# Kernel tuning notes

Hardware: AMD Instinct MI355X
Metric: run time of the kernel (lower is better)

## Reference

```python
import jax, jax.numpy as jnp
import numpy as np

K = 128          # scratch_keys_dim
A = 200          # actions_dim == scratch_values_dim
NP1 = 4          # n_pointers + 1
MAXLEN = 50      # PositionalEncoding max_len
H = K * NP1      # GRU hidden = 512


def make_pe(max_len, d):
    # Standard transformer sinusoidal positional encoding (used as scratch keys).
    pos = jnp.arange(max_len, dtype=jnp.float32)[:, None]
    div = jnp.exp(jnp.arange(0, d, 2, dtype=jnp.float32) * (-np.log(10000.0) / d))
    pe = jnp.zeros((max_len, d), jnp.float32)
    pe = pe.at[:, 0::2].set(jnp.sin(pos * div))
    pe = pe.at[:, 1::2].set(jnp.cos(pos * div))
    return pe


def setup_inputs() -> dict:
    key = jax.random.key(0)
    ks = jax.random.split(key, 12)
    B, INS, ACT = 256, 8, 33
    IN_V, OUT_V = 16, 8
    return {
        "instructions": jax.random.randint(ks[0], (INS, B), 0, IN_V, dtype=jnp.int32),
        "true_actions": jax.random.randint(ks[1], (ACT, B), 0, OUT_V, dtype=jnp.int32),
        "initial_scratch_value": jax.random.normal(ks[2], (A,), jnp.float32),
        "program_emb": jax.random.normal(ks[3], (IN_V, 200), jnp.float32) * 0.05,
        "primitive_emb": jax.random.normal(ks[4], (IN_V, A), jnp.float32) * 0.05,
        "gate_w": jax.random.normal(ks[5], (1, K), jnp.float32) * 0.05,
        "gate_b": jnp.zeros((1,), jnp.float32),
        "w_ih": jax.random.normal(ks[6], (3 * H, 1), jnp.float32) * 0.05,
        "w_hh": jax.random.normal(ks[7], (3 * H, H), jnp.float32) * 0.05,
        "b_ih": jnp.zeros((3 * H,), jnp.float32),
        "b_hh": jnp.zeros((3 * H,), jnp.float32),
        "out_w": jax.random.normal(ks[8], (OUT_V, A), jnp.float32) * 0.05,
        "out_b": jnp.zeros((OUT_V,), jnp.float32),
    }


def reference(instructions, true_actions, initial_scratch_value, program_emb,
              primitive_emb, gate_w, gate_b, w_ih, w_hh, b_ih, b_hh, out_w, out_b):
    B = instructions.shape[1]
    padded_true = true_actions[1:]              # drop BOS row, [L, B]
    L = padded_true.shape[0]                    # max_len == max_program_steps
    pe = make_pe(MAXLEN, K)
    SK = pe[:L]                                 # scratch keys [L, K] (same for all batch)
    h0 = jnp.broadcast_to(jnp.tile(pe[0], (NP1,)), (B, H))
    sv0 = jnp.broadcast_to(initial_scratch_value, (B, L, A))

    # GRU input is always zeros(B,1); compute input-side gates once.
    gi = jnp.zeros((B, 1), jnp.float32) @ w_ih.T + b_ih   # [B, 3H]

    def gru(h):
        gh = h @ w_hh.T + b_hh
        r = jax.nn.sigmoid(gi[:, :H] + gh[:, :H])
        z = jax.nn.sigmoid(gi[:, H:2 * H] + gh[:, H:2 * H])
        n = jnp.tanh(gi[:, 2 * H:] + r * gh[:, 2 * H:])
        return (1.0 - z) * n + z * h

    def word_step(carry, word):
        h, sv = carry
        prim = primitive_emb[word]              # [B, A]
        _prog = program_emb[word]               # computed but unused in original forward

        def step(c, _):
            h, sv = c
            read_p = h[:, K:2 * K]              # [B, K]
            write_p = h[:, 2 * K:3 * K]
            gate = jax.nn.sigmoid(h[:, 3 * K:4 * K] @ gate_w.T + gate_b)   # [B, 1]
            # soft read: dot-product attention over scratch keys
            read_attn = jax.nn.softmax(read_p @ SK.T, axis=-1)             # [B, L]
            read_val = jnp.einsum('bl,bla->ba', read_attn, sv)             # [B, A]
            new_val = gate * prim + (1.0 - gate) * read_val                # [B, A]
            # soft write: convex blend of new value into every slot
            wm = jax.nn.softmax(write_p @ SK.T, axis=-1)[:, :, None]       # [B, L, 1]
            sv = wm * new_val[:, None, :] + (1.0 - wm) * sv
            h = gru(h)
            return (h, sv), None

        (h, sv), _ = jax.lax.scan(step, (h, sv), None, length=L)
        return (h, sv), None

    (hF, svF), _ = jax.lax.scan(word_step, (h0, sv0), instructions)
    actions = jax.nn.log_softmax(svF @ out_w.T + out_b, axis=-1)           # [B, L, V]
    return actions.transpose(0, 2, 1), padded_true.T                       # [B,V,L], [B,L]
```

## Files before the change

### kernel.cpp

```cpp
#include <hip/hip_runtime.h>
#include <math.h>

#define NB    256
#define HDIM  512
#define LDIM  32
#define ADIM  200
#define NOUTV 8
#define NSTEP 256
#define NTHR  512
#define NWG   256
#define WPG   16
#define SCST  21

typedef __attribute__((ext_vector_type(8))) short sh8;
typedef __attribute__((ext_vector_type(4))) float f4;

union FU { uint4 u; sh8 s; };

__device__ __forceinline__ float b2f(unsigned int low16) { return __uint_as_float(low16 << 16); }

__device__ __forceinline__ void group_barrier(unsigned int* ctr, unsigned int target) {
  __syncthreads();
  if (threadIdx.x == 0) {
    __hip_atomic_fetch_add(ctr, 1u, __ATOMIC_RELEASE, __HIP_MEMORY_SCOPE_AGENT);
    while (__hip_atomic_load(ctr, __ATOMIC_ACQUIRE, __HIP_MEMORY_SCOPE_AGENT) < target) {
      __builtin_amdgcn_s_sleep(1);
    }
  }
  __syncthreads();
}

__global__ void __launch_bounds__(NTHR, 1)
sym_kernel(const int* __restrict__ instr,
           const int* __restrict__ trueact,
           const float* __restrict__ isv,
           const float* __restrict__ prim_emb,
           const float* __restrict__ gate_w,
           const float* __restrict__ gate_b,
           const float* __restrict__ w_hh,
           const float* __restrict__ b_ih,
           const float* __restrict__ b_hh,
           const float* __restrict__ out_w,
           const float* __restrict__ out_b,
           float* __restrict__ outp,
           unsigned int* __restrict__ ctrs,
           unsigned int* __restrict__ hbuf)
{
  const int tid  = threadIdx.x;
  const int wgid = blockIdx.x;
  const int x    = wgid & 7, q = wgid >> 3;
  const int gidx = x | ((q & 1) << 3);
  const int jc   = q >> 1;
  const int myb  = (gidx << 4) | jc;
  const int lane = tid & 63, wv = tid >> 6;

  __shared__ __align__(16) unsigned short sHi[16 * 512];
  __shared__ __align__(16) unsigned short sLo[16 * 512];
  __shared__ float sC[96 * SCST];
  __shared__ __align__(16) float sSV[LDIM * ADIM];
  __shared__ __align__(16) float sNV[ADIM];
  __shared__ float sSKt[128 * 32];
  __shared__ __align__(16) float sPE[16 * ADIM];
  __shared__ float sAR[LDIM], sAW[LDIM];
  __shared__ float sGate;

  unsigned int* ctr = ctrs + (gidx << 5);

  unsigned int wordpack = 0;
  #pragma unroll
  for (int wi = 0; wi < 8; ++wi)
    wordpack |= ((unsigned)instr[wi * NB + myb] & 15u) << (4 * wi);

  const int jj_t = (jc << 5) | (tid & 31);
  const float bi0 = b_ih[jj_t], bi1 = b_ih[512 + jj_t], bi2 = b_ih[1024 + jj_t];
  const float bh0 = b_hh[jj_t], bh1 = b_hh[512 + jj_t], bh2 = b_hh[1024 + jj_t];

  for (int i = tid; i < 128 * 32; i += NTHR) {
    const int k = i >> 5, l = i & 31;
    const float div = expf((float)(k & ~1) * (-9.210340371976184f / 128.0f));
    const float ang = (float)l * div;
    sSKt[i] = (k & 1) ? cosf(ang) : sinf(ang);
  }
  for (int i = tid; i < 16 * ADIM; i += NTHR) sPE[i] = prim_emb[i];
  for (int i = tid; i < LDIM * ADIM; i += NTHR) sSV[i] = isv[i % ADIM];
  {
    unsigned int* h0 = hbuf + (size_t)myb * HDIM;
    for (int k = tid; k < HDIM; k += NTHR) h0[k] = (k & 1) ? 0x3F800000u : 0u;
  }
  __syncthreads();

  unsigned int reg[128];
  if (wv < 6) {
    const int n = lane & 15, quad = lane >> 4;
    const int row96 = (wv << 4) | n;
    const int g = row96 >> 5;
    const int jj = (jc << 5) | (row96 & 31);
    const float* wrow = w_hh + (size_t)(g * 512 + jj) * 512;
    #pragma unroll
    for (int kk = 0; kk < 16; ++kk) {
      const float4 w0 = *(const float4*)(wrow + kk * 32 + quad * 8);
      const float4 w1 = *(const float4*)(wrow + kk * 32 + quad * 8 + 4);
      float e[8] = {w0.x, w0.y, w0.z, w0.w, w1.x, w1.y, w1.z, w1.w};
      unsigned int hi16[8], lo16[8];
      #pragma unroll
      for (int t = 0; t < 8; ++t) {
        const unsigned int b = __float_as_uint(e[t]);
        hi16[t] = b >> 16;
        const float rest = e[t] - __uint_as_float(b & 0xFFFF0000u);
        lo16[t] = __float_as_uint(rest) >> 16;
      }
      #pragma unroll
      for (int p = 0; p < 4; ++p) {
        reg[kk * 4 + p]      = hi16[2 * p] | (hi16[2 * p + 1] << 16);
        reg[64 + kk * 4 + p] = lo16[2 * p] | (lo16[2 * p + 1] << 16);
      }
    }
  } else if (wv == 6) {
    const int l = lane & 31;
    #pragma unroll
    for (int k = 0; k < 128; ++k) reg[k] = __float_as_uint(sSKt[k * 32 + l]);
  } else {
    reg[0] = __float_as_uint(gate_w[2 * lane]);
    reg[1] = __float_as_uint(gate_w[2 * lane + 1]);
  }

  group_barrier(ctr, WPG);

  const float gbias = gate_b[0];
  unsigned int bar = 2;

  for (int step = 0; step < NSTEP; ++step, ++bar) {
    const unsigned int* hc = hbuf + (size_t)(step & 1) * (NB * HDIM);
    unsigned int*       hn = hbuf + (size_t)((step & 1) ^ 1) * (NB * HDIM);

    {
      const uint4* src = (const uint4*)(hc + (size_t)(gidx << 4) * HDIM);
      #pragma unroll
      for (int it = 0; it < 2; ++it) {
        const int c   = tid + it * NTHR;
        const int row = c >> 6;
        const int kb  = (c & 63) << 4;
        const uint4 x0 = src[c * 2], x1 = src[c * 2 + 1];
        const int off = row * 1024 + (kb ^ ((row & 7) << 4));
        *(uint4*)((char*)sHi + off) = make_uint4(
          (x0.x >> 16) | (x0.y & 0xFFFF0000u),
          (x0.z >> 16) | (x0.w & 0xFFFF0000u),
          (x1.x >> 16) | (x1.y & 0xFFFF0000u),
          (x1.z >> 16) | (x1.w & 0xFFFF0000u));
        *(uint4*)((char*)sLo + off) = make_uint4(
          (x0.x & 0xFFFFu) | (x0.y << 16),
          (x0.z & 0xFFFFu) | (x0.w << 16),
          (x1.x & 0xFFFFu) | (x1.y << 16),
          (x1.z & 0xFFFFu) | (x1.w << 16));
      }
    }
    __syncthreads();

    if (wv < 6) {
      const int n = lane & 15, quad = lane >> 4;
      const int sw = (n & 7) << 4;
      f4 a0 = {0.f, 0.f, 0.f, 0.f}, a1 = a0, a2 = a0;
      #pragma unroll
      for (int kk = 0; kk < 16; ++kk) {
        const int off = n * 1024 + (((kk << 6) | (quad << 4)) ^ sw);
        FU fah, fal, fbh, fbl;
        fah.u = *(const uint4*)((const char*)sHi + off);
        fal.u = *(const uint4*)((const char*)sLo + off);
        fbh.u = make_uint4(reg[kk * 4], reg[kk * 4 + 1], reg[kk * 4 + 2], reg[kk * 4 + 3]);
        fbl.u = make_uint4(reg[64 + kk * 4], reg[64 + kk * 4 + 1], reg[64 + kk * 4 + 2], reg[64 + kk * 4 + 3]);
        a0 = __builtin_amdgcn_mfma_f32_16x16x32_bf16(fah.s, fbh.s, a0, 0, 0, 0);
        a1 = __builtin_amdgcn_mfma_f32_16x16x32_bf16(fah.s, fbl.s, a1, 0, 0, 0);
        a2 = __builtin_amdgcn_mfma_f32_16x16x32_bf16(fal.s, fbh.s, a2, 0, 0, 0);
      }
      const int row96 = (wv << 4) | n;
      #pragma unroll
      for (int i = 0; i < 4; ++i)
        sC[row96 * SCST + (quad << 2) + i] = a0[i] + a1[i] + a2[i];
    } else if (wv == 6) {
      const int l = lane & 31, sel = lane >> 5;
      const int sw = (jc & 7) << 4;
      float acc = 0.f;
      #pragma unroll
      for (int c = 0; c < 32; ++c) {
        const int kbyte = (128 + sel * 128 + c * 4) * 2;
        const int off = jc * 1024 + (kbyte ^ sw);
        const uint2 hb = *(const uint2*)((const char*)sHi + off);
        const uint2 lb = *(const uint2*)((const char*)sLo + off);
        const float e0 = b2f(hb.x & 0xFFFFu) + b2f(lb.x & 0xFFFFu);
        const float e1 = __uint_as_float(hb.x & 0xFFFF0000u) + __uint_as_float(lb.x & 0xFFFF0000u);
        const float e2 = b2f(hb.y & 0xFFFFu) + b2f(lb.y & 0xFFFFu);
        const float e3 = __uint_as_float(hb.y & 0xFFFF0000u) + __uint_as_float(lb.y & 0xFFFF0000u);
        acc = fmaf(e0, __uint_as_float(reg[c * 4]), acc);
        acc = fmaf(e1, __uint_as_float(reg[c * 4 + 1]), acc);
        acc = fmaf(e2, __uint_as_float(reg[c * 4 + 2]), acc);
        acc = fmaf(e3, __uint_as_float(reg[c * 4 + 3]), acc);
      }
      float mx = acc;
      #pragma unroll
      for (int m = 1; m < 32; m <<= 1) mx = fmaxf(mx, __shfl_xor(mx, m, 32));
      const float ev = __expf(acc - mx);
      float s = ev;
      #pragma unroll
      for (int m = 1; m < 32; m <<= 1) s += __shfl_xor(s, m, 32);
      (sel ? sAW : sAR)[l] = ev / s;
    } else {
      const int sw = (jc & 7) << 4;
      const int off = jc * 1024 + ((768 + 4 * lane) ^ sw);
      const unsigned int hb = *(const unsigned int*)((const char*)sHi + off);
      const unsigned int lb = *(const unsigned int*)((const char*)sLo + off);
      const float e0 = b2f(hb & 0xFFFFu) + b2f(lb & 0xFFFFu);
      const float e1 = __uint_as_float(hb & 0xFFFF0000u) + __uint_as_float(lb & 0xFFFF0000u);
      float part = fmaf(e0, __uint_as_float(reg[0]), e1 * __uint_as_float(reg[1]));
      #pragma unroll
      for (int m = 1; m < 64; m <<= 1) part += __shfl_xor(part, m, 64);
      if (lane == 0) sGate = 1.0f / (1.0f + __expf(-(part + gbias)));
    }
    __syncthreads();

    {
      const int b = tid >> 5, jcol = tid & 31;
      const float accR = sC[jcol * SCST + b];
      const float accZ = sC[(32 + jcol) * SCST + b];
      const float accN = sC[(64 + jcol) * SCST + b];
      const float r  = 1.f / (1.f + __expf(-(accR + bh0 + bi0)));
      const float z  = 1.f / (1.f + __expf(-(accZ + bh1 + bi1)));
      const float nn = tanhf(fmaf(r, accN + bh2, bi2));
      const int hoff = b * 1024 + ((jj_t * 2) ^ ((b & 7) << 4));
      const float hold = b2f(*(const unsigned short*)((const char*)sHi + hoff))
                       + b2f(*(const unsigned short*)((const char*)sLo + hoff));
      const float hnew = fmaf(z, hold - nn, nn);
      const unsigned int hibits = __float_as_uint(hnew) & 0xFFFF0000u;
      const float rest = hnew - __uint_as_float(hibits);
      const unsigned int lobits = __float_as_uint(rest) >> 16;
      hn[(size_t)((gidx << 4) + b) * HDIM + jj_t] = hibits | lobits;
    }
    if (tid < ADIM) {
      const int word = (wordpack >> ((step >> 5) << 2)) & 15u;
      float rv = 0.f;
      #pragma unroll 8
      for (int l = 0; l < LDIM; ++l) rv = fmaf(sAR[l], sSV[l * ADIM + tid], rv);
      const float g = sGate;
      sNV[tid] = fmaf(g, sPE[word * ADIM + tid], (1.f - g) * rv);
    }
    __syncthreads();

    {
      const f4* nv4 = (const f4*)sNV;
      f4* sv4 = (f4*)sSV;
      #pragma unroll
      for (int it = 0; it < 4; ++it) {
        const int s4 = tid + it * NTHR;
        if (s4 < 1600) {
          const int l = s4 / 50, a4 = s4 - l * 50;
          const float w = sAW[l];
          const f4 nv = nv4[a4];
          f4 sv = sv4[s4];
          sv.x = fmaf(w, nv.x - sv.x, sv.x);
          sv.y = fmaf(w, nv.y - sv.y, sv.y);
          sv.z = fmaf(w, nv.z - sv.z, sv.z);
          sv.w = fmaf(w, nv.w - sv.w, sv.w);
          sv4[s4] = sv;
        }
      }
    }

    group_barrier(ctr, bar * WPG);
  }

  if (tid < 256) {
    const int l = tid >> 3, v = tid & 7;
    const float* svrow = sSV + l * ADIM;
    const float* wrow  = out_w + v * ADIM;
    float acc = out_b[v];
    #pragma unroll 8
    for (int a = 0; a < ADIM; ++a) acc = fmaf(svrow[a], wrow[a], acc);
    float mx = acc;
    #pragma unroll
    for (int m = 1; m < 8; m <<= 1) mx = fmaxf(mx, __shfl_xor(mx, m, 8));
    const float e = __expf(acc - mx);
    float s = e;
    #pragma unroll
    for (int m = 1; m < 8; m <<= 1) s += __shfl_xor(s, m, 8);
    outp[(size_t)myb * (NOUTV * LDIM) + v * LDIM + l] = acc - mx - logf(s);
  }
  if (tid < LDIM) {
    outp[NB * NOUTV * LDIM + myb * LDIM + tid] = (float)trueact[(tid + 1) * NB + myb];
  }
}

extern "C" void kernel_launch(void* const* d_in, const int* in_sizes, int n_in,
                              void* d_out, int out_size, void* d_ws, size_t ws_size,
                              hipStream_t stream) {
  const int*   instr   = (const int*)d_in[0];
  const int*   trueact = (const int*)d_in[1];
  const float* isv     = (const float*)d_in[2];
  const float* prim    = (const float*)d_in[4];
  const float* gate_w  = (const float*)d_in[5];
  const float* gate_b  = (const float*)d_in[6];
  const float* w_hh    = (const float*)d_in[8];
  const float* b_ih    = (const float*)d_in[9];
  const float* b_hh    = (const float*)d_in[10];
  const float* out_w   = (const float*)d_in[11];
  const float* out_b   = (const float*)d_in[12];
  float* outp = (float*)d_out;

  unsigned int* ctrs = (unsigned int*)d_ws;
  unsigned int* hbuf = (unsigned int*)((char*)d_ws + 4096);

  hipMemsetAsync(d_ws, 0, 4096, stream);

  void* args[] = { (void*)&instr, (void*)&trueact, (void*)&isv, (void*)&prim,
                   (void*)&gate_w, (void*)&gate_b, (void*)&w_hh, (void*)&b_ih,
                   (void*)&b_hh, (void*)&out_w, (void*)&out_b, (void*)&outp,
                   (void*)&ctrs, (void*)&hbuf };
  hipLaunchCooperativeKernel((const void*)sym_kernel, dim3(NWG), dim3(NTHR),
                             args, 0, stream);
}
```

Before: 2.076 ms.

## Replace counter barrier with per-workgroup flag slots and keep scratch in registers

Swaps the shared atomic-counter group barrier for per-workgroup release flags. Each workgroup publishes its step number as soon as its h slice is written, then one wave polls all 16 slots with a ballot while the other threads update the scratch memory. The 32x200 scratch values now live in per-thread registers, fused into a single read-and-write pass that removes the shared-memory sweep and one __syncthreads per step. The attention dot product is also split across four accumulators to shorten its dependency chain. The cost is higher register pressure on top of the 128-entry reg array, which risks spills, and different ordering semantics in the barrier.

```diff
diff --git a/kernel.cpp b/kernel.cpp
--- a/kernel.cpp
+++ b/kernel.cpp
@@ -9,8 +9,8 @@
 #define NSTEP 256
 #define NTHR  512
 #define NWG   256
-#define WPG   16
 #define SCST  21
+#define SLOT(m) ((((m) & 3) << 4) | ((m) >> 2))
 
 typedef __attribute__((ext_vector_type(8))) short sh8;
 typedef __attribute__((ext_vector_type(4))) float f4;
@@ -18,17 +18,6 @@
 union FU { uint4 u; sh8 s; };
 
 __device__ __forceinline__ float b2f(unsigned int low16) { return __uint_as_float(low16 << 16); }
-
-__device__ __forceinline__ void group_barrier(unsigned int* ctr, unsigned int target) {
-  __syncthreads();
-  if (threadIdx.x == 0) {
-    __hip_atomic_fetch_add(ctr, 1u, __ATOMIC_RELEASE, __HIP_MEMORY_SCOPE_AGENT);
-    while (__hip_atomic_load(ctr, __ATOMIC_ACQUIRE, __HIP_MEMORY_SCOPE_AGENT) < target) {
-      __builtin_amdgcn_s_sleep(1);
-    }
-  }
-  __syncthreads();
-}
 
 __global__ void __launch_bounds__(NTHR, 1)
 sym_kernel(const int* __restrict__ instr,
@@ -57,14 +46,14 @@
   __shared__ __align__(16) unsigned short sHi[16 * 512];
   __shared__ __align__(16) unsigned short sLo[16 * 512];
   __shared__ float sC[96 * SCST];
-  __shared__ __align__(16) float sSV[LDIM * ADIM];
-  __shared__ __align__(16) float sNV[ADIM];
   __shared__ float sSKt[128 * 32];
   __shared__ __align__(16) float sPE[16 * ADIM];
-  __shared__ float sAR[LDIM], sAW[LDIM];
+  __shared__ __align__(16) float sAR[LDIM];
+  __shared__ __align__(16) float sAW[LDIM];
   __shared__ float sGate;
-
-  unsigned int* ctr = ctrs + (gidx << 5);
+  __shared__ __align__(16) float sSVe[LDIM * ADIM];
+
+  unsigned int* slots = ctrs + (gidx << 6);
 
   unsigned int wordpack = 0;
   #pragma unroll
@@ -82,7 +71,13 @@
     sSKt[i] = (k & 1) ? cosf(ang) : sinf(ang);
   }
   for (int i = tid; i < 16 * ADIM; i += NTHR) sPE[i] = prim_emb[i];
-  for (int i = tid; i < LDIM * ADIM; i += NTHR) sSV[i] = isv[i % ADIM];
+
+  float sv[LDIM];
+  {
+    const float v = (tid < ADIM) ? isv[tid] : 0.f;
+    #pragma unroll
+    for (int l = 0; l < LDIM; ++l) sv[l] = v;
+  }
   {
     unsigned int* h0 = hbuf + (size_t)myb * HDIM;
     for (int k = tid; k < HDIM; k += NTHR) h0[k] = (k & 1) ? 0x3F800000u : 0u;
@@ -124,12 +119,24 @@
     reg[1] = __float_as_uint(gate_w[2 * lane + 1]);
   }
 
-  group_barrier(ctr, WPG);
+  __syncthreads();
+  if (tid == 448)
+    __hip_atomic_store(&slots[SLOT(jc)], 1u, __ATOMIC_RELEASE, __HIP_MEMORY_SCOPE_AGENT);
+  if (wv == 7) {
+    bool done;
+    do {
+      unsigned int v = (lane < 16)
+        ? __hip_atomic_load(&slots[SLOT(lane)], __ATOMIC_ACQUIRE, __HIP_MEMORY_SCOPE_AGENT) : 1u;
+      done = (__ballot(v >= 1u) == ~0ull);
+      if (!done) __builtin_amdgcn_s_sleep(1);
+    } while (!done);
+  }
+  __syncthreads();
 
   const float gbias = gate_b[0];
-  unsigned int bar = 2;
-
-  for (int step = 0; step < NSTEP; ++step, ++bar) {
+
+  for (int step = 0; step < NSTEP; ++step) {
+    const unsigned int bar = step + 2;
     const unsigned int* hc = hbuf + (size_t)(step & 1) * (NB * HDIM);
     unsigned int*       hn = hbuf + (size_t)((step & 1) ^ 1) * (NB * HDIM);
 
@@ -179,22 +186,21 @@
     } else if (wv == 6) {
       const int l = lane & 31, sel = lane >> 5;
       const int sw = (jc & 7) << 4;
-      float acc = 0.f;
+      float ac0 = 0.f, ac1 = 0.f, ac2 = 0.f, ac3 = 0.f;
       #pragma unroll
       for (int c = 0; c < 32; ++c) {
         const int kbyte = (128 + sel * 128 + c * 4) * 2;
         const int off = jc * 1024 + (kbyte ^ sw);
         const uint2 hb = *(const uint2*)((const char*)sHi + off);
         const uint2 lb = *(const uint2*)((const char*)sLo + off);
-        const float e0 = b2f(hb.x & 0xFFFFu) + b2f(lb.x & 0xFFFFu);
-        const float e1 = __uint_as_float(hb.x & 0xFFFF0000u) + __uint_as_float(lb.x & 0xFFFF0000u);
-        const float e2 = b2f(hb.y & 0xFFFFu) + b2f(lb.y & 0xFFFFu);
-        const float e3 = __uint_as_float(hb.y & 0xFFFF0000u) + __uint_as_float(lb.y & 0xFFFF0000u);
-        acc = fmaf(e0, __uint_as_float(reg[c * 4]), acc);
-        acc = fmaf(e1, __uint_as_float(reg[c * 4 + 1]), acc);
-        acc = fmaf(e2, __uint_as_float(reg[c * 4 + 2]), acc);
-        acc = fmaf(e3, __uint_as_float(reg[c * 4 + 3]), acc);
-      }
+        ac0 = fmaf(b2f(hb.x & 0xFFFFu) + b2f(lb.x & 0xFFFFu), __uint_as_float(reg[c * 4]), ac0);
+        ac1 = fmaf(__uint_as_float(hb.x & 0xFFFF0000u) + __uint_as_float(lb.x & 0xFFFF0000u),
+                   __uint_as_float(reg[c * 4 + 1]), ac1);
+        ac2 = fmaf(b2f(hb.y & 0xFFFFu) + b2f(lb.y & 0xFFFFu), __uint_as_float(reg[c * 4 + 2]), ac2);
+        ac3 = fmaf(__uint_as_float(hb.y & 0xFFFF0000u) + __uint_as_float(lb.y & 0xFFFF0000u),
+                   __uint_as_float(reg[c * 4 + 3]), ac3);
+      }
+      float acc = (ac0 + ac1) + (ac2 + ac3);
       float mx = acc;
       #pragma unroll
       for (int m = 1; m < 32; m <<= 1) mx = fmaxf(mx, __shfl_xor(mx, m, 32));
@@ -234,42 +240,56 @@
       const unsigned int lobits = __float_as_uint(rest) >> 16;
       hn[(size_t)((gidx << 4) + b) * HDIM + jj_t] = hibits | lobits;
     }
+    __syncthreads();
+
+    if (tid == 448)
+      __hip_atomic_store(&slots[SLOT(jc)], bar, __ATOMIC_RELEASE, __HIP_MEMORY_SCOPE_AGENT);
+
     if (tid < ADIM) {
       const int word = (wordpack >> ((step >> 5) << 2)) & 15u;
+      const float g = sGate;
+      const float pv = sPE[word * ADIM + tid];
       float rv = 0.f;
-      #pragma unroll 8
-      for (int l = 0; l < LDIM; ++l) rv = fmaf(sAR[l], sSV[l * ADIM + tid], rv);
-      const float g = sGate;
-      sNV[tid] = fmaf(g, sPE[word * ADIM + tid], (1.f - g) * rv);
+      const f4* ar4 = (const f4*)sAR;
+      #pragma unroll
+      for (int j = 0; j < 8; ++j) {
+        const f4 a = ar4[j];
+        rv = fmaf(a.x, sv[4 * j],     rv);
+        rv = fmaf(a.y, sv[4 * j + 1], rv);
+        rv = fmaf(a.z, sv[4 * j + 2], rv);
+        rv = fmaf(a.w, sv[4 * j + 3], rv);
+      }
+      const float nv = fmaf(g, pv, (1.f - g) * rv);
+      const f4* aw4 = (const f4*)sAW;
+      #pragma unroll
+      for (int j = 0; j < 8; ++j) {
+        const f4 w = aw4[j];
+        sv[4 * j]     = fmaf(w.x, nv - sv[4 * j],     sv[4 * j]);
+        sv[4 * j + 1] = fmaf(w.y, nv - sv[4 * j + 1], sv[4 * j + 1]);
+        sv[4 * j + 2] = fmaf(w.z, nv - sv[4 * j + 2], sv[4 * j + 2]);
+        sv[4 * j + 3] = fmaf(w.w, nv - sv[4 * j + 3], sv[4 * j + 3]);
+      }
+    } else if (wv == 7) {
+      bool done;
+      do {
+        unsigned int v = (lane < 16)
+          ? __hip_atomic_load(&slots[SLOT(lane)], __ATOMIC_ACQUIRE, __HIP_MEMORY_SCOPE_AGENT) : bar;
+        done = (__ballot(v >= bar) == ~0ull);
+        if (!done) __builtin_amdgcn_s_sleep(1);
+      } while (!done);
     }
     __syncthreads();
-
-    {
-      const f4* nv4 = (const f4*)sNV;
-      f4* sv4 = (f4*)sSV;
-      #pragma unroll
-      for (int it = 0; it < 4; ++it) {
-        const int s4 = tid + it * NTHR;
-        if (s4 < 1600) {
-          const int l = s4 / 50, a4 = s4 - l * 50;
-          const float w = sAW[l];
-          const f4 nv = nv4[a4];
-          f4 sv = sv4[s4];
-          sv.x = fmaf(w, nv.x - sv.x, sv.x);
-          sv.y = fmaf(w, nv.y - sv.y, sv.y);
-          sv.z = fmaf(w, nv.z - sv.z, sv.z);
-          sv.w = fmaf(w, nv.w - sv.w, sv.w);
-          sv4[s4] = sv;
-        }
-      }
-    }
-
-    group_barrier(ctr, bar * WPG);
-  }
+  }
+
+  if (tid < ADIM) {
+    #pragma unroll
+    for (int l = 0; l < LDIM; ++l) sSVe[l * ADIM + tid] = sv[l];
+  }
+  __syncthreads();
 
   if (tid < 256) {
     const int l = tid >> 3, v = tid & 7;
-    const float* svrow = sSV + l * ADIM;
+    const float* svrow = sSVe + l * ADIM;
     const float* wrow  = out_w + v * ADIM;
     float acc = out_b[v];
     #pragma unroll 8
```

Result: slower. 4.601 ms (+121.6%).
